# Performance work log

Hardware: AMD Instinct MI355X
Metric: run time of the kernel (lower is better)

The kernel has to match this reference:

```python
import jax, jax.numpy as jnp
import numpy as np

B, C_IN, C_OUT, N, K = 8, 64, 128, 2048, 16
EPS = 1e-5  # torch BatchNorm2d default


def setup_inputs() -> dict:
    key = jax.random.key(0)
    ks = jax.random.split(key, 2)
    x = jax.random.normal(ks[0], (B, C_IN, N, 1), dtype=jnp.float32)
    # Conv2d(2*C_IN, C_OUT, 1) kaiming_normal weight, zero bias; 1x1 kernel -> [C_OUT, 2*C_IN]
    W = jax.random.normal(ks[1], (C_OUT, 2 * C_IN), dtype=jnp.float32) * np.float32(np.sqrt(2.0 / (2 * C_IN)))
    b = jnp.zeros((C_OUT,), jnp.float32)
    gamma = jnp.ones((C_OUT,), jnp.float32)   # BN weight filled with 1
    beta = jnp.zeros((C_OUT,), jnp.float32)   # BN bias zeroed
    return {"x": x, "W": W, "b": b, "gamma": gamma, "beta": beta, "k": K}


def reference(x, W, b, gamma, beta, k):
    # x: [B, C, N, 1]
    xs = x[..., 0]                              # [B, C, N]
    feats = jnp.transpose(xs, (0, 2, 1))        # [B, N, C]
    # knn: pairwise_distance = -||xi||^2 + 2 xi.xj - ||xj||^2 (negative sq dist)
    sq = jnp.sum(xs * xs, axis=1)               # [B, N]
    gram = jnp.einsum('bcn,bcm->bnm', xs, xs)   # [B, N, N]
    pd = 2.0 * gram - sq[:, :, None] - sq[:, None, :]
    idx = jax.lax.top_k(pd, k)[1]               # [B, N, k] neighbor indices
    # gather: x_j = neighbor features, x_i = center features broadcast over k
    x_j = jnp.take_along_axis(feats[:, None, :, :], idx[:, :, :, None], axis=2)  # [B, N, k, C]
    x_i = feats[:, :, None, :]                  # [B, N, 1, C]
    e = jnp.concatenate([jnp.broadcast_to(x_i, x_j.shape), x_j - x_i], axis=-1)  # [B, N, k, 2C]
    # 1x1 conv (matmul over channels) + ReLU
    h = jax.nn.relu(jnp.einsum('bnkc,oc->bnko', e, W) + b)  # [B, N, k, O]
    # BatchNorm2d in training mode: batch stats over (B, N, k), biased variance
    mean = jnp.mean(h, axis=(0, 1, 2))
    var = jnp.mean(jnp.square(h - mean), axis=(0, 1, 2))
    h = (h - mean) * jax.lax.rsqrt(var + EPS) * gamma + beta
    # max over neighbors, back to [B, O, N, 1]
    out = jnp.max(h, axis=2)                    # [B, N, O]
    return jnp.transpose(out, (0, 2, 1))[..., None]
```

## Files before the change

### kernel.cpp

```cpp
#include <hip/hip_runtime.h>
#include <math.h>

#define BB 8
#define CIN 64
#define CO 128
#define NPT 2048
#define KK 16
#define EPSV 1e-5f
#define LOSCALE 2048.0f

typedef unsigned int u32;
typedef unsigned long long u64;
typedef _Float16 f16x8 __attribute__((ext_vector_type(8)));
typedef float f32x4 __attribute__((ext_vector_type(4)));

__global__ __launch_bounds__(256) void k_prep_pv(
    const float* __restrict__ x, const float* __restrict__ W,
    const float* __restrict__ bias, float* __restrict__ sq,
    _Float16* __restrict__ xh, _Float16* __restrict__ xl,
    float* __restrict__ p, float* __restrict__ v) {
  __shared__ float tile[64][65];
  __shared__ float tileT[64][68];
  __shared__ float psum[4][64];
  int bid = blockIdx.x;
  int b = bid >> 5;
  int n0 = (bid & 31) << 6;
  int tid = threadIdx.x;
  int q = tid >> 6, lo = tid & 63;
#pragma unroll
  for (int i = 0; i < 16; ++i) {
    int c = i * 4 + q;
    tile[c][lo] = x[((size_t)(b * CIN + c)) * NPT + n0 + lo];
  }
  __syncthreads();
  float ps = 0.f;
#pragma unroll
  for (int i = 0; i < 16; ++i) {
    float t = tile[q * 16 + i][lo];
    ps += t * t;
  }
  psum[q][lo] = ps;
#pragma unroll
  for (int i = 0; i < 16; ++i) {
    int ni = i * 4 + q;
    float val = tile[lo][ni];
    tileT[ni][lo] = val;
    size_t o = ((size_t)(b * NPT + n0 + ni)) * CIN + lo;
    _Float16 h = (_Float16)val;
    xh[o] = h;
    xl[o] = (_Float16)((val - (float)h) * LOSCALE);
  }
  __syncthreads();
  if (q == 0) {
    sq[(size_t)b * NPT + n0 + lo] = psum[0][lo] + psum[1][lo] + psum[2][lo] + psum[3][lo];
  }
  int o = tid & 127, hh = tid >> 7;
  const float4* W1 = (const float4*)&W[o * 2 * CIN];
  const float4* W2 = (const float4*)&W[o * 2 * CIN + CIN];
  float bo = bias[o];
#pragma unroll 1
  for (int t = 0; t < 32; ++t) {
    int node = t * 2 + hh;
    float a1 = 0.f, a2 = 0.f;
#pragma unroll
    for (int c4 = 0; c4 < 16; ++c4) {
      float4 xv = *(const float4*)&tileT[node][c4 * 4];
      float4 w1 = W1[c4];
      float4 w2 = W2[c4];
      a1 += xv.x * w1.x + xv.y * w1.y + xv.z * w1.z + xv.w * w1.w;
      a2 += xv.x * w2.x + xv.y * w2.y + xv.z * w2.z + xv.w * w2.w;
    }
    size_t gn = ((size_t)(b * NPT + n0 + node)) * CO + o;
    p[gn] = a1 - a2 + bo;
    v[gn] = a2;
  }
}

__global__ __launch_bounds__(1024) void k_dist_topk(
    const _Float16* __restrict__ xh, const _Float16* __restrict__ xl,
    const float* __restrict__ sq, int* __restrict__ idxout) {
  __shared__ uint4 tiles[16][2][256];
  __shared__ float submax[16][64];
  __shared__ float2 cand[16][96];
  __shared__ int cnt[16];
  __shared__ float tauf[16];

  int bid = (blockIdx.x & 7) * 128 + (blockIdx.x >> 3);
  int b = bid >> 7;
  int rt = (bid & 127) << 4;
  int tid = threadIdx.x;
  int w = tid >> 6, lane = tid & 63;
  int lr = lane & 15, lg = lane >> 4;
  const _Float16* xhb = xh + (size_t)b * NPT * CIN;
  const _Float16* xlb = xl + (size_t)b * NPT * CIN;
  const float* sqb = sq + (size_t)b * NPT;

  if (tid < 16) cnt[tid] = 0;

  const size_t arow = (size_t)(rt + lr) * CIN + lg * 8;
  f16x8 ah0 = *(const f16x8*)(xhb + arow);
  f16x8 ah1 = *(const f16x8*)(xhb + arow + 32);
  f16x8 al0 = *(const f16x8*)(xlb + arow);
  f16x8 al1 = *(const f16x8*)(xlb + arow + 32);
  float4 sqr = *(const float4*)(sqb + rt + lg * 4);
  float sqrv[4] = {sqr.x, sqr.y, sqr.z, sqr.w};
  float csqs[8];
#pragma unroll
  for (int t = 0; t < 8; ++t) csqs[t] = sqb[(w * 8 + t) * 16 + lr];

  const char* xhB = (const char*)xhb;
  const char* xlB = (const char*)xlb;
  const int su = (lane ^ ((lane >> 3) & 7)) * 16;

#define ISSUE_TILE(T)                                                          \
  {                                                                            \
    const int tb_ = (w * 8 + (T)) * 2048;                                      \
    uint4* buf_ = &tiles[w][(T) & 1][0];                                       \
    __builtin_amdgcn_global_load_lds((const uint4*)(xhB + tb_ + su),           \
                                     buf_, 16, 0, 0);                          \
    __builtin_amdgcn_global_load_lds((const uint4*)(xhB + tb_ + 1024 + su),    \
                                     buf_ + 64, 16, 0, 0);                     \
    __builtin_amdgcn_global_load_lds((const uint4*)(xlB + tb_ + su),           \
                                     buf_ + 128, 16, 0, 0);                    \
    __builtin_amdgcn_global_load_lds((const uint4*)(xlB + tb_ + 1024 + su),    \
                                     buf_ + 192, 16, 0, 0);                    \
  }

  ISSUE_TILE(0)
  ISSUE_TILE(1)

  const int uh0 = lr * 8 + (lg ^ (lr & 7));
  const int uh1 = lr * 8 + ((lg + 4) ^ (lr & 7));
  float vals[32];

#pragma unroll
  for (int t = 0; t < 8; ++t) {
    if (t < 7) { asm volatile("s_waitcnt vmcnt(4)" ::: "memory"); }
    else       { asm volatile("s_waitcnt vmcnt(0)" ::: "memory"); }
    __builtin_amdgcn_sched_barrier(0);
    const uint4* bufr = &tiles[w][t & 1][0];
    f16x8 bh0 = *(const f16x8*)(bufr + uh0);
    f16x8 bh1 = *(const f16x8*)(bufr + uh1);
    f16x8 bl0 = *(const f16x8*)(bufr + 128 + uh0);
    f16x8 bl1 = *(const f16x8*)(bufr + 128 + uh1);
    f32x4 acc0 = {0.f, 0.f, 0.f, 0.f};
    f32x4 acc1 = {0.f, 0.f, 0.f, 0.f};
    acc1 = __builtin_amdgcn_mfma_f32_16x16x32_f16(ah0, bl0, acc1, 0, 0, 0);
    acc1 = __builtin_amdgcn_mfma_f32_16x16x32_f16(al0, bh0, acc1, 0, 0, 0);
    acc1 = __builtin_amdgcn_mfma_f32_16x16x32_f16(ah1, bl1, acc1, 0, 0, 0);
    acc1 = __builtin_amdgcn_mfma_f32_16x16x32_f16(al1, bh1, acc1, 0, 0, 0);
    acc0 = __builtin_amdgcn_mfma_f32_16x16x32_f16(ah0, bh0, acc0, 0, 0, 0);
    acc0 = __builtin_amdgcn_mfma_f32_16x16x32_f16(ah1, bh1, acc0, 0, 0, 0);
    const float k2 = 2.0f / LOSCALE;
#pragma unroll
    for (int q = 0; q < 4; ++q) {
      vals[t * 4 + q] = fmaf(acc1[q], k2, 2.f * acc0[q]) - (sqrv[q] + csqs[t]);
    }
    asm volatile("s_waitcnt lgkmcnt(0)" ::: "memory");
    __builtin_amdgcn_sched_barrier(0);
    if (t == 0) ISSUE_TILE(2)
    if (t == 1) ISSUE_TILE(3)
    if (t == 2) ISSUE_TILE(4)
    if (t == 3) ISSUE_TILE(5)
    if (t == 4) ISSUE_TILE(6)
    if (t == 5) ISSUE_TILE(7)
  }
#undef ISSUE_TILE

  float rmax[4];
#pragma unroll
  for (int q = 0; q < 4; ++q) {
    float m = vals[q];
#pragma unroll
    for (int t = 1; t < 8; ++t) m = fmaxf(m, vals[t * 4 + q]);
    m = fmaxf(m, __shfl_xor(m, 1, 64));
    m = fmaxf(m, __shfl_xor(m, 2, 64));
    rmax[q] = m;
  }
  if ((lr & 3) == 0) {
    int pool = w * 4 + (lr >> 2);
#pragma unroll
    for (int q = 0; q < 4; ++q) submax[lg * 4 + q][pool] = rmax[q];
  }
  __syncthreads();

  {
    u32 ou = __float_as_uint(submax[w][lane]);
    ou = (ou & 0x80000000u) ? ~ou : (ou | 0x80000000u);
    u32 lo = 0u;
#pragma unroll
    for (int s2 = 31; s2 >= 16; --s2) {
      u32 cd = lo | (1u << s2);
      u64 bal = __ballot(ou >= cd);
      if (__popcll(bal) >= KK) lo = cd;
    }
    u32 tb = (lo & 0x80000000u) ? (lo ^ 0x80000000u) : ~lo;
    if (lane == 0) tauf[w] = __uint_as_float(tb);
  }
  __syncthreads();

  {
    float tq[4];
#pragma unroll
    for (int q = 0; q < 4; ++q) tq[q] = tauf[lg * 4 + q];
#pragma unroll
    for (int t = 0; t < 8; ++t) {
#pragma unroll
      for (int q = 0; q < 4; ++q) {
        float vv = vals[t * 4 + q];
        if (vv >= tq[q]) {
          int r = lg * 4 + q;
          int pos = atomicAdd(&cnt[r], 1);
          if (pos < 96) cand[r][pos] = make_float2(vv, __int_as_float((w * 8 + t) * 16 + lr));
        }
      }
    }
  }
  __syncthreads();

  int total = cnt[w];
  if (total > 96) total = 96;
  const float NINF = -__builtin_inff();
  float cv = NINF;
  int ci = 0x7FFFFFFF;
  int n1 = total < 64 ? total : 64;
  if (lane < n1) {
    float2 pr = cand[w][lane];
    cv = pr.x; ci = __float_as_int(pr.y);
  }

#define PSORT(KMAX)                                                        \
  _Pragma("unroll") for (int k = 2; k <= (KMAX); k <<= 1) {                \
    _Pragma("unroll") for (int j = k >> 1; j > 0; j >>= 1) {               \
      float pv = __shfl_xor(cv, j, 64);                                    \
      int pi = __shfl_xor(ci, j, 64);                                      \
      bool up = (lane & k) != 0;                                           \
      bool lw = (lane & j) == 0;                                           \
      bool gt = (cv > pv) || (cv == pv && ci < pi);                        \
      bool keep = (lw != up) ? gt : !gt;                                   \
      cv = keep ? cv : pv;                                                 \
      ci = keep ? ci : pi;                                                 \
    }                                                                      \
  }

  if (total > 32) {
    PSORT(64)
    if (total > 64) {
      if (lane >= 16) {
        int src2 = 48 + lane;
        if (src2 < total) {
          float2 pr = cand[w][src2];
          cv = pr.x; ci = __float_as_int(pr.y);
        } else { cv = NINF; ci = 0x7FFFFFFF; }
      }
      PSORT(64)
    }
  } else {
    PSORT(32)
  }
#undef PSORT

  if (lane < KK) idxout[((size_t)(b * NPT + rt + w)) * KK + lane] = ci;
}

__global__ __launch_bounds__(256) void k_stats(
    float* p_mn, const float* __restrict__ v, const int* __restrict__ idx,
    float* __restrict__ psums, float* __restrict__ psqs, float* __restrict__ mxb) {
  __shared__ float rs[8][CO];
  __shared__ float rq[8][CO];
  int bid = (blockIdx.x & 7) * 64 + (blockIdx.x >> 3);
  int b = bid >> 6;
  int n0 = (bid & 63) << 5;
  int tid = threadIdx.x;
  int o4 = tid & 31, ns = tid >> 5;
  const float* vb = v + (size_t)b * NPT * CO;
  float4 s = {0.f, 0.f, 0.f, 0.f};
  float4 qq = {0.f, 0.f, 0.f, 0.f};
#pragma unroll 1
  for (int g = 0; g < 4; ++g) {
    int gn = b * NPT + n0 + g * 8 + ns;
    size_t po = (size_t)gn * CO + o4 * 4;
    float4 p4 = *(const float4*)(p_mn + po);
    const int* id = idx + (size_t)gn * KK;
    int4 j0 = *(const int4*)(id);
    int4 j1 = *(const int4*)(id + 4);
    int4 j2 = *(const int4*)(id + 8);
    int4 j3 = *(const int4*)(id + 12);
    int jj[16] = {j0.x, j0.y, j0.z, j0.w, j1.x, j1.y, j1.z, j1.w,
                  j2.x, j2.y, j2.z, j2.w, j3.x, j3.y, j3.z, j3.w};
    float4 mx4 = {-1e30f, -1e30f, -1e30f, -1e30f};
    float4 mn4 = {1e30f, 1e30f, 1e30f, 1e30f};
#pragma unroll
    for (int k = 0; k < KK; ++k) {
      float4 v4 = *(const float4*)(vb + (size_t)jj[k] * CO + o4 * 4);
      float h0 = fmaxf(p4.x + v4.x, 0.f);
      float h1 = fmaxf(p4.y + v4.y, 0.f);
      float h2 = fmaxf(p4.z + v4.z, 0.f);
      float h3 = fmaxf(p4.w + v4.w, 0.f);
      s.x += h0; s.y += h1; s.z += h2; s.w += h3;
      qq.x += h0 * h0; qq.y += h1 * h1; qq.z += h2 * h2; qq.w += h3 * h3;
      mx4.x = fmaxf(mx4.x, h0); mx4.y = fmaxf(mx4.y, h1);
      mx4.z = fmaxf(mx4.z, h2); mx4.w = fmaxf(mx4.w, h3);
      mn4.x = fminf(mn4.x, h0); mn4.y = fminf(mn4.y, h1);
      mn4.z = fminf(mn4.z, h2); mn4.w = fminf(mn4.w, h3);
    }
    *(float4*)(mxb + po) = mx4;
    *(float4*)(p_mn + po) = mn4;
  }
  rs[ns][o4 * 4 + 0] = s.x;  rs[ns][o4 * 4 + 1] = s.y;
  rs[ns][o4 * 4 + 2] = s.z;  rs[ns][o4 * 4 + 3] = s.w;
  rq[ns][o4 * 4 + 0] = qq.x; rq[ns][o4 * 4 + 1] = qq.y;
  rq[ns][o4 * 4 + 2] = qq.z; rq[ns][o4 * 4 + 3] = qq.w;
  __syncthreads();
  if (tid < CO) {
    float ts = 0.f, tq = 0.f;
#pragma unroll
    for (int i = 0; i < 8; ++i) { ts += rs[i][tid]; tq += rq[i][tid]; }
    psums[(size_t)bid * CO + tid] = ts;
    psqs[(size_t)bid * CO + tid] = tq;
  }
}

__global__ __launch_bounds__(64) void k_final(
    const float* __restrict__ psums, const float* __restrict__ psqs,
    const float* __restrict__ gamma, const float* __restrict__ beta,
    float* __restrict__ scale, float* __restrict__ shift) {
  int o = blockIdx.x;
  int t = threadIdx.x;
  float s = 0.f, q = 0.f;
  for (int i = t; i < BB * (NPT / 32); i += 64) {
    s += psums[(size_t)i * CO + o];
    q += psqs[(size_t)i * CO + o];
  }
#pragma unroll
  for (int d = 32; d >= 1; d >>= 1) {
    s += __shfl_down(s, d, 64);
    q += __shfl_down(q, d, 64);
  }
  if (t == 0) {
    const float M = (float)(BB * NPT * KK);
    float mean = s / M;
    float var = q / M - mean * mean;
    float sc = gamma[o] * rsqrtf(var + EPSV);
    scale[o] = sc;
    shift[o] = beta[o] - mean * sc;
  }
}

__global__ __launch_bounds__(256) void k_out_fast(
    const float* __restrict__ mxb, const float* __restrict__ mnb,
    const float* __restrict__ scale, const float* __restrict__ shift,
    float* __restrict__ out) {
  __shared__ float ob[32][132];
  int bid = blockIdx.x;
  int b = bid >> 6;
  int n0 = (bid & 63) << 5;
  int tid = threadIdx.x;
  int o4 = tid & 31, ns = tid >> 5;
  float4 sc = *(const float4*)(scale + o4 * 4);
  float4 sh = *(const float4*)(shift + o4 * 4);
#pragma unroll
  for (int g = 0; g < 4; ++g) {
    int node = g * 8 + ns;
    size_t po = (size_t)(b * NPT + n0 + node) * CO + o4 * 4;
    float4 mx = *(const float4*)(mxb + po);
    float4 mn = *(const float4*)(mnb + po);
    float4 r;
    r.x = (sc.x >= 0.f ? mx.x : mn.x) * sc.x + sh.x;
    r.y = (sc.y >= 0.f ? mx.y : mn.y) * sc.y + sh.y;
    r.z = (sc.z >= 0.f ? mx.z : mn.z) * sc.z + sh.z;
    r.w = (sc.w >= 0.f ? mx.w : mn.w) * sc.w + sh.w;
    *(float4*)&ob[node][o4 * 4] = r;
  }
  __syncthreads();
  int ni = tid & 31, oh = tid >> 5;
#pragma unroll
  for (int pass = 0; pass < 16; ++pass) {
    int o = pass * 8 + oh;
    out[((size_t)(b * CO + o)) * NPT + n0 + ni] = ob[ni][o];
  }
}

extern "C" void kernel_launch(void* const* d_in, const int* in_sizes, int n_in,
                              void* d_out, int out_size, void* d_ws, size_t ws_size,
                              hipStream_t stream) {
  const float* x = (const float*)d_in[0];
  const float* W = (const float*)d_in[1];
  const float* bias = (const float*)d_in[2];
  const float* gamma = (const float*)d_in[3];
  const float* beta = (const float*)d_in[4];
  float* out = (float*)d_out;

  char* ws = (char*)d_ws;
  size_t off = 0;
  auto alloc = [&](size_t bytes) {
    void* ptr = ws + off;
    off += (bytes + 255) & ~(size_t)255;
    return ptr;
  };
  float* ft = (float*)alloc(sizeof(float) * BB * NPT * CIN);
  _Float16* xh = (_Float16*)alloc(sizeof(_Float16) * BB * NPT * CIN);
  _Float16* xl = (_Float16*)alloc(sizeof(_Float16) * BB * NPT * CIN);
  float* mx = ft;
  float* sq = (float*)alloc(sizeof(float) * BB * NPT);
  float* p = (float*)alloc(sizeof(float) * BB * NPT * CO);
  float* v = (float*)alloc(sizeof(float) * BB * NPT * CO);
  int* idx = (int*)alloc(sizeof(int) * BB * NPT * KK);
  float* psums = (float*)alloc(sizeof(float) * BB * (NPT / 32) * CO);
  float* psqs = (float*)alloc(sizeof(float) * BB * (NPT / 32) * CO);
  float* scale = (float*)alloc(sizeof(float) * CO);
  float* shift = (float*)alloc(sizeof(float) * CO);
  (void)ws_size; (void)in_sizes; (void)n_in; (void)out_size;

  hipLaunchKernelGGL(k_prep_pv, dim3(BB * (NPT / 64)), dim3(256), 0, stream,
                     x, W, bias, sq, xh, xl, p, v);
  hipLaunchKernelGGL(k_dist_topk, dim3(BB * (NPT / 16)), dim3(1024), 0, stream, xh, xl, sq, idx);
  hipLaunchKernelGGL(k_stats, dim3(BB * (NPT / 32)), dim3(256), 0, stream, p, v, idx, psums, psqs, mx);
  hipLaunchKernelGGL(k_final, dim3(CO), dim3(64), 0, stream, psums, psqs, gamma, beta, scale, shift);
  hipLaunchKernelGGL(k_out_fast, dim3(BB * (NPT / 32)), dim3(256), 0, stream, mx, p, scale, shift, out);
}
```

Measured before the change: 113.5 us.

## Split prep/pv kernels, radix-select top-k via ballots, double stats grid

Splits the fused prep+projection kernel into a transpose/split kernel that writes fp32 features and a separate projection kernel with 4x more blocks, raising parallelism for the per-node W matmul. Replaces the bitonic shuffle sort in top-k with a ballot-based radix select over packed 64-bit distance/index keys, and enlarges the candidate buffer to 128. Halves nodes per block in the stats kernel to double its grid. These changes add an extra kernel launch and an fp32 feature round trip through global memory. The top-k output order also changes, becoming unsorted by distance.

After: 136.3 us. 20.1% more time.

```diff
diff --git a/kernel.cpp b/kernel.cpp
--- a/kernel.cpp
+++ b/kernel.cpp
@@ -14,13 +14,16 @@
 typedef _Float16 f16x8 __attribute__((ext_vector_type(8)));
 typedef float f32x4 __attribute__((ext_vector_type(4)));
 
-__global__ __launch_bounds__(256) void k_prep_pv(
-    const float* __restrict__ x, const float* __restrict__ W,
-    const float* __restrict__ bias, float* __restrict__ sq,
-    _Float16* __restrict__ xh, _Float16* __restrict__ xl,
-    float* __restrict__ p, float* __restrict__ v) {
+__device__ __forceinline__ u64 packdm(float f, int m) {
+  u32 u = __float_as_uint(f);
+  u = (u & 0x80000000u) ? ~u : (u | 0x80000000u);
+  return ((u64)u << 32) | (u64)(0xFFFFFFFFu - (u32)m);
+}
+
+__global__ __launch_bounds__(256) void k_prep(
+    const float* __restrict__ x, float* __restrict__ ft, float* __restrict__ sq,
+    _Float16* __restrict__ xh, _Float16* __restrict__ xl) {
   __shared__ float tile[64][65];
-  __shared__ float tileT[64][68];
   __shared__ float psum[4][64];
   int bid = blockIdx.x;
   int b = bid >> 5;
@@ -44,8 +47,8 @@
   for (int i = 0; i < 16; ++i) {
     int ni = i * 4 + q;
     float val = tile[lo][ni];
-    tileT[ni][lo] = val;
     size_t o = ((size_t)(b * NPT + n0 + ni)) * CIN + lo;
+    ft[o] = val;
     _Float16 h = (_Float16)val;
     xh[o] = h;
     xl[o] = (_Float16)((val - (float)h) * LOSCALE);
@@ -54,17 +57,33 @@
   if (q == 0) {
     sq[(size_t)b * NPT + n0 + lo] = psum[0][lo] + psum[1][lo] + psum[2][lo] + psum[3][lo];
   }
+}
+
+__global__ __launch_bounds__(256) void k_pv(
+    const float* __restrict__ ft, const float* __restrict__ W,
+    const float* __restrict__ bias, float* __restrict__ p, float* __restrict__ v) {
+  __shared__ float xn[16][68];
+  int bid = (blockIdx.x & 7) * 128 + (blockIdx.x >> 3);
+  int b = bid >> 7;
+  int n0 = (bid & 127) << 4;
+  int tid = threadIdx.x;
+  {
+    int node = tid >> 4, c4 = (tid & 15) * 4;
+    float4 t4 = *(const float4*)(ft + ((size_t)(b * NPT + n0 + node)) * CIN + c4);
+    *(float4*)&xn[node][c4] = t4;
+  }
+  __syncthreads();
   int o = tid & 127, hh = tid >> 7;
   const float4* W1 = (const float4*)&W[o * 2 * CIN];
   const float4* W2 = (const float4*)&W[o * 2 * CIN + CIN];
   float bo = bias[o];
-#pragma unroll 1
-  for (int t = 0; t < 32; ++t) {
+#pragma unroll 2
+  for (int t = 0; t < 8; ++t) {
     int node = t * 2 + hh;
     float a1 = 0.f, a2 = 0.f;
 #pragma unroll
     for (int c4 = 0; c4 < 16; ++c4) {
-      float4 xv = *(const float4*)&tileT[node][c4 * 4];
+      float4 xv = *(const float4*)&xn[node][c4 * 4];
       float4 w1 = W1[c4];
       float4 w2 = W2[c4];
       a1 += xv.x * w1.x + xv.y * w1.y + xv.z * w1.z + xv.w * w1.w;
@@ -81,7 +100,7 @@
     const float* __restrict__ sq, int* __restrict__ idxout) {
   __shared__ uint4 tiles[16][2][256];
   __shared__ float submax[16][64];
-  __shared__ float2 cand[16][96];
+  __shared__ float2 cand[16][128];
   __shared__ int cnt[16];
   __shared__ float tauf[16];
 
@@ -211,7 +230,7 @@
         if (vv >= tq[q]) {
           int r = lg * 4 + q;
           int pos = atomicAdd(&cnt[r], 1);
-          if (pos < 96) cand[r][pos] = make_float2(vv, __int_as_float((w * 8 + t) * 16 + lr));
+          if (pos < 128) cand[r][pos] = make_float2(vv, __int_as_float((w * 8 + t) * 16 + lr));
         }
       }
     }
@@ -219,48 +238,39 @@
   __syncthreads();
 
   int total = cnt[w];
-  if (total > 96) total = 96;
-  const float NINF = -__builtin_inff();
-  float cv = NINF;
-  int ci = 0x7FFFFFFF;
-  int n1 = total < 64 ? total : 64;
-  if (lane < n1) {
+  if (total > 128) total = 128;
+  u64 k1 = 0, k2 = 0;
+  int ci1 = 0, ci2 = 0;
+  if (lane < total) {
     float2 pr = cand[w][lane];
-    cv = pr.x; ci = __float_as_int(pr.y);
-  }
-
-#define PSORT(KMAX)                                                        \
-  _Pragma("unroll") for (int k = 2; k <= (KMAX); k <<= 1) {                \
-    _Pragma("unroll") for (int j = k >> 1; j > 0; j >>= 1) {               \
-      float pv = __shfl_xor(cv, j, 64);                                    \
-      int pi = __shfl_xor(ci, j, 64);                                      \
-      bool up = (lane & k) != 0;                                           \
-      bool lw = (lane & j) == 0;                                           \
-      bool gt = (cv > pv) || (cv == pv && ci < pi);                        \
-      bool keep = (lw != up) ? gt : !gt;                                   \
-      cv = keep ? cv : pv;                                                 \
-      ci = keep ? ci : pi;                                                 \
-    }                                                                      \
-  }
-
-  if (total > 32) {
-    PSORT(64)
-    if (total > 64) {
-      if (lane >= 16) {
-        int src2 = 48 + lane;
-        if (src2 < total) {
-          float2 pr = cand[w][src2];
-          cv = pr.x; ci = __float_as_int(pr.y);
-        } else { cv = NINF; ci = 0x7FFFFFFF; }
-      }
-      PSORT(64)
-    }
-  } else {
-    PSORT(32)
-  }
-#undef PSORT
-
-  if (lane < KK) idxout[((size_t)(b * NPT + rt + w)) * KK + lane] = ci;
+    ci1 = __float_as_int(pr.y);
+    k1 = packdm(pr.x, ci1);
+  }
+  if (64 + lane < total) {
+    float2 pr = cand[w][64 + lane];
+    ci2 = __float_as_int(pr.y);
+    k2 = packdm(pr.x, ci2);
+  }
+  u64 lo = 0;
+#pragma unroll
+  for (int s2 = 63; s2 >= 32; --s2) {
+    u64 cd = lo | (1ull << s2);
+    int c = __popcll(__ballot(k1 >= cd)) + __popcll(__ballot(k2 >= cd));
+    if (c >= KK) lo = cd;
+  }
+  lo |= 0xFFFFF800ull;
+#pragma unroll
+  for (int s2 = 10; s2 >= 0; --s2) {
+    u64 cd = lo | (1ull << s2);
+    int c = __popcll(__ballot(k1 >= cd)) + __popcll(__ballot(k2 >= cd));
+    if (c >= KK) lo = cd;
+  }
+  u64 m1 = __ballot(k1 >= lo);
+  u64 m2 = __ballot(k2 >= lo);
+  const u64 below = (lane == 0) ? 0ull : (~0ull >> (64 - lane));
+  int* myout = idxout + ((size_t)(b * NPT + rt + w)) * KK;
+  if (k1 >= lo) myout[(int)__popcll(m1 & below)] = ci1;
+  if (k2 >= lo) myout[(int)__popcll(m1) + (int)__popcll(m2 & below)] = ci2;
 }
 
 __global__ __launch_bounds__(256) void k_stats(
@@ -268,16 +278,16 @@
     float* __restrict__ psums, float* __restrict__ psqs, float* __restrict__ mxb) {
   __shared__ float rs[8][CO];
   __shared__ float rq[8][CO];
-  int bid = (blockIdx.x & 7) * 64 + (blockIdx.x >> 3);
-  int b = bid >> 6;
-  int n0 = (bid & 63) << 5;
+  int bid = (blockIdx.x & 7) * 128 + (blockIdx.x >> 3);
+  int b = bid >> 7;
+  int n0 = (bid & 127) << 4;
   int tid = threadIdx.x;
   int o4 = tid & 31, ns = tid >> 5;
   const float* vb = v + (size_t)b * NPT * CO;
   float4 s = {0.f, 0.f, 0.f, 0.f};
   float4 qq = {0.f, 0.f, 0.f, 0.f};
 #pragma unroll 1
-  for (int g = 0; g < 4; ++g) {
+  for (int g = 0; g < 2; ++g) {
     int gn = b * NPT + n0 + g * 8 + ns;
     size_t po = (size_t)gn * CO + o4 * 4;
     float4 p4 = *(const float4*)(p_mn + po);
@@ -328,7 +338,7 @@
   int o = blockIdx.x;
   int t = threadIdx.x;
   float s = 0.f, q = 0.f;
-  for (int i = t; i < BB * (NPT / 32); i += 64) {
+  for (int i = t; i < BB * (NPT / 16); i += 64) {
     s += psums[(size_t)i * CO + o];
     q += psqs[(size_t)i * CO + o];
   }
@@ -406,16 +416,16 @@
   float* p = (float*)alloc(sizeof(float) * BB * NPT * CO);
   float* v = (float*)alloc(sizeof(float) * BB * NPT * CO);
   int* idx = (int*)alloc(sizeof(int) * BB * NPT * KK);
-  float* psums = (float*)alloc(sizeof(float) * BB * (NPT / 32) * CO);
-  float* psqs = (float*)alloc(sizeof(float) * BB * (NPT / 32) * CO);
+  float* psums = (float*)alloc(sizeof(float) * BB * (NPT / 16) * CO);
+  float* psqs = (float*)alloc(sizeof(float) * BB * (NPT / 16) * CO);
   float* scale = (float*)alloc(sizeof(float) * CO);
   float* shift = (float*)alloc(sizeof(float) * CO);
   (void)ws_size; (void)in_sizes; (void)n_in; (void)out_size;
 
-  hipLaunchKernelGGL(k_prep_pv, dim3(BB * (NPT / 64)), dim3(256), 0, stream,
-                     x, W, bias, sq, xh, xl, p, v);
+  hipLaunchKernelGGL(k_prep, dim3(BB * (NPT / 64)), dim3(256), 0, stream, x, ft, sq, xh, xl);
+  hipLaunchKernelGGL(k_pv, dim3(BB * (NPT / 16)), dim3(256), 0, stream, ft, W, bias, p, v);
   hipLaunchKernelGGL(k_dist_topk, dim3(BB * (NPT / 16)), dim3(1024), 0, stream, xh, xl, sq, idx);
-  hipLaunchKernelGGL(k_stats, dim3(BB * (NPT / 32)), dim3(256), 0, stream, p, v, idx, psums, psqs, mx);
+  hipLaunchKernelGGL(k_stats, dim3(BB * (NPT / 16)), dim3(256), 0, stream, p, v, idx, psums, psqs, mx);
   hipLaunchKernelGGL(k_final, dim3(CO), dim3(64), 0, stream, psums, psqs, gamma, beta, scale, shift);
   hipLaunchKernelGGL(k_out_fast, dim3(BB * (NPT / 32)), dim3(256), 0, stream, mx, p, scale, shift, out);
 }
```
